# Kernel optimization log

Hardware: AMD Instinct MI355X
Metric: run time of the kernel (lower is better)

Reference implementation:

```python
import jax, jax.numpy as jnp
import numpy as np

N = 10000      # num_nodes
E = 320000     # num_edges
B = 8          # batch
S = 12         # seq_length
H = 64         # hidden_channels
HEADS = 4
C = H // HEADS # per-head dim = 16
L = 3          # num_layers
P = 3          # pred_length
EPS = 1e-5


def setup_inputs():
    key = jax.random.key(0)
    ks = jax.random.split(key, 20)
    g = lambda k, sh, s=0.05: jax.random.normal(k, sh, dtype=jnp.float32) * s
    return {
        "x": jax.random.normal(ks[0], (B, S, N), dtype=jnp.float32),
        "edge_index": jax.random.randint(ks[1], (2, E), 0, N, dtype=jnp.int64),
        "in_W": g(ks[2], (S, H), 0.2), "in_b": g(ks[3], (H,)),
        "Wq": g(ks[4], (L, H, H), 0.1), "bq": g(ks[5], (L, H)),
        "Wk": g(ks[6], (L, H, H), 0.1), "bk": g(ks[7], (L, H)),
        "Wv": g(ks[8], (L, H, H), 0.1), "bv": g(ks[9], (L, H)),
        "Wsk": g(ks[10], (L, H, H), 0.1), "bsk": g(ks[11], (L, H)),
        "ln_g": jnp.ones((H,), jnp.float32), "ln_b": jnp.zeros((H,), jnp.float32),
        "out_W": g(ks[12], (H, P), 0.1), "out_b": g(ks[13], (P,)),
    }


def _layer_norm(x, g, b):
    mu = x.mean(-1, keepdims=True)
    var = ((x - mu) ** 2).mean(-1, keepdims=True)
    return (x - mu) * jax.lax.rsqrt(var + EPS) * g + b


def _transformer_conv(x, src, dst, Wq, bq, Wk, bk, Wv, bv, Wsk, bsk):
    # x: [N, H]; PyG TransformerConv, concat=True, root_weight=True, beta=False
    n = x.shape[0]
    q = (x @ Wq + bq).reshape(n, HEADS, C)
    k = (x @ Wk + bk).reshape(n, HEADS, C)
    v = (x @ Wv + bv).reshape(n, HEADS, C)
    # messages flow src -> dst; attention logits per edge per head
    logits = (q[dst] * k[src]).sum(-1) / np.sqrt(C)           # [E, HEADS]
    m = jax.ops.segment_max(logits, dst, num_segments=n)       # [N, HEADS]
    e = jnp.exp(logits - m[dst])
    den = jax.ops.segment_sum(e, dst, num_segments=n)          # [N, HEADS]
    a = e / den[dst]                                           # [E, HEADS]
    agg = jax.ops.segment_sum(a[..., None] * v[src], dst, num_segments=n)
    return agg.reshape(n, H) + x @ Wsk + bsk


def reference(x, edge_index, in_W, in_b, Wq, bq, Wk, bk, Wv, bv, Wsk, bsk,
              ln_g, ln_b, out_W, out_b):
    src, dst = edge_index[0], edge_index[1]
    h = jnp.einsum('bsn,sh->bnh', x, in_W) + in_b              # [B, N, H]
    for l in range(L):
        conv = jax.vmap(lambda xb: _transformer_conv(
            xb, src, dst, Wq[l], bq[l], Wk[l], bk[l],
            Wv[l], bv[l], Wsk[l], bsk[l]))(h)
        h = _layer_norm(h + conv, ln_g, ln_b)                  # dropout: eval mode
    out = h @ out_W + out_b                                    # [B, N, P]
    return out.transpose(0, 2, 1)                              # [B, P, N]
```

## Files before the change

### kernel.cpp

```cpp
#include <hip/hip_runtime.h>
#include <hip/hip_bf16.h>
#include <math.h>

#define NN 10000
#define EE 320000
#define BB 8
#define SS 12
#define PP 3
#define LL 3
#define BN (BB*NN)
#define CSR_CAP (EE + 16*NN + 64)
#define QSCL (0.25f * 1.44269504f)

typedef __attribute__((ext_vector_type(8))) short bf8_t;
typedef __attribute__((ext_vector_type(4))) float f4_t;

__device__ __forceinline__ float bf2f(unsigned short u) {
    unsigned int x = ((unsigned int)u) << 16;
    return __builtin_bit_cast(float, x);
}
__device__ __forceinline__ unsigned short f2bf(float f) {
    unsigned int u = __builtin_bit_cast(unsigned int, f);
    u += 0x7FFF + ((u >> 16) & 1);
    return (unsigned short)(u >> 16);
}
__device__ __forceinline__ unsigned short f2h(float f) {
    _Float16 h = (_Float16)f;
    return __builtin_bit_cast(unsigned short, h);
}
__device__ __forceinline__ float dot2(unsigned a, unsigned b, float c) {
    float d;
    asm("v_dot2_f32_f16 %0, %1, %2, %3" : "=v"(d) : "v"(a), "v"(b), "v"(c));
    return d;
}
__device__ __forceinline__ float fma_mixlo(unsigned v, float w, float acc) {
    float d;
    asm("v_fma_mix_f32 %0, %1, %2, %3 op_sel_hi:[1,0,0]"
        : "=v"(d) : "v"(v), "v"(w), "v"(acc));
    return d;
}
__device__ __forceinline__ float fma_mixhi(unsigned v, float w, float acc) {
    float d;
    asm("v_fma_mix_f32 %0, %1, %2, %3 op_sel:[1,0,0] op_sel_hi:[1,0,0]"
        : "=v"(d) : "v"(v), "v"(w), "v"(acc));
    return d;
}
template<int CTRL>
__device__ __forceinline__ float dppadd(float x) {
    int t = __builtin_amdgcn_update_dpp(0, __builtin_bit_cast(int, x), CTRL, 0xF, 0xF, true);
    return x + __builtin_bit_cast(float, t);
}
#define QX1 0xB1
#define QX2 0x4E
#define RR4 0x124
#define RR8 0x128
__device__ __forceinline__ float quad_sum(float x) {
    x = dppadd<QX1>(x); x = dppadd<QX2>(x); return x;
}
__device__ __forceinline__ float row_sum(float x) {
    x = dppadd<QX1>(x); x = dppadd<QX2>(x);
    x = dppadd<RR4>(x); x = dppadd<RR8>(x); return x;
}

__global__ __launch_bounds__(256) void k_count(const int* __restrict__ ei, int* __restrict__ cnt,
                                               const float* __restrict__ Wq, const float* __restrict__ Wk,
                                               const float* __restrict__ Wv, const float* __restrict__ Ws,
                                               const float* __restrict__ bq, const float* __restrict__ bk,
                                               const float* __restrict__ bv, const float* __restrict__ bs,
                                               unsigned short* __restrict__ wtb, float* __restrict__ bprep) {
    int e = blockIdx.x * 256 + threadIdx.x;
    if (e < EE) atomicAdd(&cnt[ei[EE + e]], 1);
    if (e < LL * 4 * 64 * 64) {
        int l = e >> 14; int j = (e >> 12) & 3; int col = (e >> 6) & 63; int k = e & 63;
        const float* W = (j == 0 ? Wq : j == 1 ? Wk : j == 2 ? Wv : Ws) + l * 4096;
        float v = W[k * 64 + col];
        if (j == 0) v *= QSCL;
        wtb[e] = f2bf(v);
    }
    if (e < LL * 4 * 64) {
        int l = e >> 8; int j = (e >> 6) & 3; int c = e & 63;
        const float* bsrc = (j == 0 ? bq : j == 1 ? bk : j == 2 ? bv : bs) + l * 64;
        bprep[e] = bsrc[c] * (j == 0 ? QSCL : 1.0f);
    }
}

__global__ __launch_bounds__(1024) void k_scan(int* __restrict__ cnt,
                                               int* __restrict__ rp,
                                               int* __restrict__ degv) {
    __shared__ int ssum[1024];
    int t = threadIdx.x;
    int base = t * 10;
    int loc[10];
    int s = 0;
#pragma unroll
    for (int j = 0; j < 10; ++j) {
        int i = base + j;
        int d = (i < NN) ? cnt[i] : 0;
        loc[j] = d;
        s += (d + 15) & ~15;
    }
    ssum[t] = s;
    __syncthreads();
    for (int off = 1; off < 1024; off <<= 1) {
        int v = (t >= off) ? ssum[t - off] : 0;
        __syncthreads();
        ssum[t] += v;
        __syncthreads();
    }
    int run = ssum[t] - s;
#pragma unroll
    for (int j = 0; j < 10; ++j) {
        int i = base + j;
        if (i < NN) {
            rp[i]   = run;
            degv[i] = loc[j];
            cnt[i]  = run;
            run += (loc[j] + 15) & ~15;
        }
    }
}

__global__ __launch_bounds__(256) void k_fill(const int* __restrict__ ei, int* __restrict__ cursor,
                                              int* __restrict__ csr) {
    int e = blockIdx.x * 256 + threadIdx.x;
    if (e >= EE) return;
    int dst = ei[EE + e];
    int pos = atomicAdd(&cursor[dst], 1);
    csr[pos] = ei[e] << 8;
}

__global__ __launch_bounds__(256, 4) void k_gemm(const float* __restrict__ x,
                                                 const float* __restrict__ inW,
                                                 const float* __restrict__ inb,
                                                 int first,
                                                 unsigned short* hb,
                                                 float* h,
                                                 const unsigned short* __restrict__ wtb,
                                                 const float* __restrict__ bprep,
                                                 unsigned short* __restrict__ qh,
                                                 unsigned short* __restrict__ kv) {
    int tid = threadIdx.x;
    int l = tid & 63, w = tid >> 6;
    int row0 = blockIdx.x * 64;
    int colb = l & 15, kg = l >> 4, rquad = kg;

    if (first) {
        int c = tid & 63;
        int rb = tid >> 6;
        for (int j = 0; j < 16; ++j) {
            int row = row0 + rb + j * 4;
            int b = row / NN;
            int n = row - b * NN;
            float s = inb[c];
#pragma unroll
            for (int t = 0; t < SS; ++t)
                s += x[((size_t)b * SS + t) * NN + n] * inW[t * 64 + c];
            h[(size_t)row * 64 + c]  = s;
            hb[(size_t)row * 64 + c] = f2bf(s);
        }
        __syncthreads();
    }

    const unsigned short* wb = wtb + (size_t)w * 4096;
    bf8_t wfr[2][4];
#pragma unroll
    for (int ks = 0; ks < 2; ++ks)
#pragma unroll
        for (int ct = 0; ct < 4; ++ct)
            wfr[ks][ct] = *(const bf8_t*)(wb + (ct * 16 + colb) * 64 + ks * 32 + kg * 8);
    float4 biasv[4];
#pragma unroll
    for (int ct = 0; ct < 4; ++ct)
        biasv[ct] = *(const float4*)(bprep + w * 64 + ct * 16 + rquad * 4);

#pragma unroll
    for (int rt = 0; rt < 4; ++rt) {
        bf8_t hfr[2];
#pragma unroll
        for (int ks = 0; ks < 2; ++ks)
            hfr[ks] = *(const bf8_t*)(hb + (size_t)(row0 + rt * 16 + colb) * 64 + ks * 32 + kg * 8);
        f4_t acc[4];
#pragma unroll
        for (int ct = 0; ct < 4; ++ct) acc[ct] = (f4_t){0.f, 0.f, 0.f, 0.f};
#pragma unroll
        for (int ks = 0; ks < 2; ++ks)
#pragma unroll
            for (int ct = 0; ct < 4; ++ct)
                acc[ct] = __builtin_amdgcn_mfma_f32_16x16x32_bf16(wfr[ks][ct], hfr[ks], acc[ct], 0, 0, 0);

        int rowid = row0 + rt * 16 + colb;
        size_t rowoff = (size_t)rowid * 64;
#pragma unroll
        for (int ct = 0; ct < 4; ++ct) {
            int c0 = ct * 16 + rquad * 4;
            float v0 = acc[ct][0] + biasv[ct].x;
            float v1 = acc[ct][1] + biasv[ct].y;
            float v2 = acc[ct][2] + biasv[ct].z;
            float v3 = acc[ct][3] + biasv[ct].w;
            if (w == 0) {
                ushort4 st = {f2h(v0), f2h(v1), f2h(v2), f2h(v3)};
                *(ushort4*)(qh + rowoff + c0) = st;
            } else if (w == 1) {
                ushort4 st = {f2h(v0), f2h(v1), f2h(v2), f2h(v3)};
                *(ushort4*)(kv + (size_t)rowid * 128 + ((c0 >> 2) << 3)) = st;
            } else if (w == 2) {
                ushort4 st = {f2h(v0), f2h(v1), f2h(v2), f2h(v3)};
                *(ushort4*)(kv + (size_t)rowid * 128 + ((c0 >> 2) << 3) + 4) = st;
            } else {
                float4 hv = *(float4*)(h + rowoff + c0);
                hv.x += v0; hv.y += v1; hv.z += v2; hv.w += v3;
                *(float4*)(h + rowoff + c0) = hv;
            }
        }
    }
}

__global__ __launch_bounds__(256, 8) void k_attn_ln(const unsigned short* __restrict__ qh,
                                                    const unsigned short* __restrict__ kv,
                                                    const int* __restrict__ rp,
                                                    const int* __restrict__ degv,
                                                    const int* __restrict__ csr,
                                                    const float* __restrict__ lng,
                                                    const float* __restrict__ lnb,
                                                    float* __restrict__ h,
                                                    unsigned short* __restrict__ hb,
                                                    const float* __restrict__ oW,
                                                    const float* __restrict__ ob,
                                                    float* __restrict__ out) {
    int b    = blockIdx.x & 7;
    int n    = ((blockIdx.x >> 3) << 2) | __builtin_amdgcn_readfirstlane(threadIdx.x >> 6);
    int lane = threadIdx.x & 63;
    int lg   = lane & 15;
    int grp  = lane >> 4;
    size_t wid = (size_t)b * NN + n;

    const char* kvbase = (const char*)kv + (size_t)b * NN * 256;
    int lgoff = lg * 16;

    uint2 qp = ((const uint2*)qh)[wid * 16 + lg];

    int e0 = rp[n], deg = degv[n];
    int nf  = deg >> 4;
    int rem = deg & 15;
    float den0 = 0.f, den1 = 0.f;
    float4 av0 = {0.f, 0.f, 0.f, 0.f}, av1 = {0.f, 0.f, 0.f, 0.f};

    int e = e0;
    for (int f = 0; f < nf; ++f, e += 16) {
        int4 cc = *(const int4*)(csr + e + grp * 4);
        unsigned o0 = (unsigned)(cc.x + lgoff);
        unsigned o1 = (unsigned)(cc.y + lgoff);
        unsigned o2 = (unsigned)(cc.z + lgoff);
        unsigned o3 = (unsigned)(cc.w + lgoff);
        uint4 a0 = *(const uint4*)(kvbase + o0);
        uint4 a1 = *(const uint4*)(kvbase + o1);
        uint4 a2 = *(const uint4*)(kvbase + o2);
        uint4 a3 = *(const uint4*)(kvbase + o3);

        float d0 = dot2(a0.y, qp.y, dot2(a0.x, qp.x, 0.f));
        float d1 = dot2(a1.y, qp.y, dot2(a1.x, qp.x, 0.f));
        float d2 = dot2(a2.y, qp.y, dot2(a2.x, qp.x, 0.f));
        float d3 = dot2(a3.y, qp.y, dot2(a3.x, qp.x, 0.f));
        d0 = quad_sum(d0); d1 = quad_sum(d1);
        d2 = quad_sum(d2); d3 = quad_sum(d3);

        float w0 = __builtin_amdgcn_exp2f(d0);
        float w1 = __builtin_amdgcn_exp2f(d1);
        float w2 = __builtin_amdgcn_exp2f(d2);
        float w3 = __builtin_amdgcn_exp2f(d3);

        den0 += w0 + w1;
        den1 += w2 + w3;
        av0.x = fma_mixlo(a0.z, w0, av0.x); av0.x = fma_mixlo(a1.z, w1, av0.x);
        av0.y = fma_mixhi(a0.z, w0, av0.y); av0.y = fma_mixhi(a1.z, w1, av0.y);
        av0.z = fma_mixlo(a0.w, w0, av0.z); av0.z = fma_mixlo(a1.w, w1, av0.z);
        av0.w = fma_mixhi(a0.w, w0, av0.w); av0.w = fma_mixhi(a1.w, w1, av0.w);
        av1.x = fma_mixlo(a2.z, w2, av1.x); av1.x = fma_mixlo(a3.z, w3, av1.x);
        av1.y = fma_mixhi(a2.z, w2, av1.y); av1.y = fma_mixhi(a3.z, w3, av1.y);
        av1.z = fma_mixlo(a2.w, w2, av1.z); av1.z = fma_mixlo(a3.w, w3, av1.z);
        av1.w = fma_mixhi(a2.w, w2, av1.w); av1.w = fma_mixhi(a3.w, w3, av1.w);
    }
    if (rem) {
        int4 cc = *(const int4*)(csr + e + grp * 4);
        unsigned o0 = (unsigned)(cc.x + lgoff);
        unsigned o1 = (unsigned)(cc.y + lgoff);
        unsigned o2 = (unsigned)(cc.z + lgoff);
        unsigned o3 = (unsigned)(cc.w + lgoff);
        uint4 a0 = *(const uint4*)(kvbase + o0);
        uint4 a1 = *(const uint4*)(kvbase + o1);
        uint4 a2 = *(const uint4*)(kvbase + o2);
        uint4 a3 = *(const uint4*)(kvbase + o3);

        int eb = grp * 4;
        float m0 = (eb + 0 < rem) ? 1.f : 0.f;
        float m1 = (eb + 1 < rem) ? 1.f : 0.f;
        float m2 = (eb + 2 < rem) ? 1.f : 0.f;
        float m3 = (eb + 3 < rem) ? 1.f : 0.f;

        float d0 = dot2(a0.y, qp.y, dot2(a0.x, qp.x, 0.f));
        float d1 = dot2(a1.y, qp.y, dot2(a1.x, qp.x, 0.f));
        float d2 = dot2(a2.y, qp.y, dot2(a2.x, qp.x, 0.f));
        float d3 = dot2(a3.y, qp.y, dot2(a3.x, qp.x, 0.f));
        d0 = quad_sum(d0); d1 = quad_sum(d1);
        d2 = quad_sum(d2); d3 = quad_sum(d3);

        float w0 = m0 * __builtin_amdgcn_exp2f(d0);
        float w1 = m1 * __builtin_amdgcn_exp2f(d1);
        float w2 = m2 * __builtin_amdgcn_exp2f(d2);
        float w3 = m3 * __builtin_amdgcn_exp2f(d3);

        den0 += w0 + w1;
        den1 += w2 + w3;
        av0.x = fma_mixlo(a0.z, w0, av0.x); av0.x = fma_mixlo(a1.z, w1, av0.x);
        av0.y = fma_mixhi(a0.z, w0, av0.y); av0.y = fma_mixhi(a1.z, w1, av0.y);
        av0.z = fma_mixlo(a0.w, w0, av0.z); av0.z = fma_mixlo(a1.w, w1, av0.z);
        av0.w = fma_mixhi(a0.w, w0, av0.w); av0.w = fma_mixhi(a1.w, w1, av0.w);
        av1.x = fma_mixlo(a2.z, w2, av1.x); av1.x = fma_mixlo(a3.z, w3, av1.x);
        av1.y = fma_mixhi(a2.z, w2, av1.y); av1.y = fma_mixhi(a3.z, w3, av1.y);
        av1.z = fma_mixlo(a2.w, w2, av1.z); av1.z = fma_mixlo(a3.w, w3, av1.z);
        av1.w = fma_mixhi(a2.w, w2, av1.w); av1.w = fma_mixhi(a3.w, w3, av1.w);
    }

    float den = den0 + den1;
    float4 av = {av0.x + av1.x, av0.y + av1.y, av0.z + av1.z, av0.w + av1.w};

#pragma unroll
    for (int off = 16; off <= 32; off <<= 1) {
        den  += __shfl_xor(den, off);
        av.x += __shfl_xor(av.x, off); av.y += __shfl_xor(av.y, off);
        av.z += __shfl_xor(av.z, off); av.w += __shfl_xor(av.w, off);
    }
    float inv = (den > 0.f) ? __builtin_amdgcn_rcpf(den) : 0.f;

    float4 h4 = ((const float4*)h)[wid * 16 + lg];
    float4 x4;
    x4.x = h4.x + av.x * inv; x4.y = h4.y + av.y * inv;
    x4.z = h4.z + av.z * inv; x4.w = h4.w + av.w * inv;

    float s = row_sum(x4.x + x4.y + x4.z + x4.w);
    float mu = s * (1.f / 64.f);
    float4 dx;
    dx.x = x4.x - mu; dx.y = x4.y - mu; dx.z = x4.z - mu; dx.w = x4.w - mu;
    float vs = row_sum(dx.x * dx.x + dx.y * dx.y + dx.z * dx.z + dx.w * dx.w);
    float r = __builtin_amdgcn_rsqf(vs * (1.f / 64.f) + 1e-5f);

    float4 g4 = ((const float4*)lng)[lg];
    float4 b4 = ((const float4*)lnb)[lg];
    float4 o4;
    o4.x = dx.x * r * g4.x + b4.x; o4.y = dx.y * r * g4.y + b4.y;
    o4.z = dx.z * r * g4.z + b4.z; o4.w = dx.w * r * g4.w + b4.w;

    if (oW) {
        int c0 = lg * 4;
        float t0 = o4.x * oW[(c0+0)*3+0] + o4.y * oW[(c0+1)*3+0] + o4.z * oW[(c0+2)*3+0] + o4.w * oW[(c0+3)*3+0];
        float t1 = o4.x * oW[(c0+0)*3+1] + o4.y * oW[(c0+1)*3+1] + o4.z * oW[(c0+2)*3+1] + o4.w * oW[(c0+3)*3+1];
        float t2 = o4.x * oW[(c0+0)*3+2] + o4.y * oW[(c0+1)*3+2] + o4.z * oW[(c0+2)*3+2] + o4.w * oW[(c0+3)*3+2];
        t0 = row_sum(t0); t1 = row_sum(t1); t2 = row_sum(t2);
        if (lane == 0) {
            out[((size_t)b * PP + 0) * NN + n] = t0 + ob[0];
            out[((size_t)b * PP + 1) * NN + n] = t1 + ob[1];
            out[((size_t)b * PP + 2) * NN + n] = t2 + ob[2];
        }
    } else if (lane < 16) {
        ((float4*)h)[wid * 16 + lg] = o4;
        ushort4 hu = {f2bf(o4.x), f2bf(o4.y), f2bf(o4.z), f2bf(o4.w)};
        ((ushort4*)hb)[wid * 16 + lg] = hu;
    }
}

extern "C" void kernel_launch(void* const* d_in, const int* in_sizes, int n_in,
                              void* d_out, int out_size, void* d_ws, size_t ws_size,
                              hipStream_t stream) {
    const float* x    = (const float*)d_in[0];
    const int*   ei   = (const int*)  d_in[1];
    const float* inW  = (const float*)d_in[2];
    const float* inb  = (const float*)d_in[3];
    const float* Wq   = (const float*)d_in[4];
    const float* bq   = (const float*)d_in[5];
    const float* Wk   = (const float*)d_in[6];
    const float* bk   = (const float*)d_in[7];
    const float* Wv   = (const float*)d_in[8];
    const float* bv   = (const float*)d_in[9];
    const float* Wsk  = (const float*)d_in[10];
    const float* bsk  = (const float*)d_in[11];
    const float* lng  = (const float*)d_in[12];
    const float* lnb  = (const float*)d_in[13];
    const float* outW = (const float*)d_in[14];
    const float* outb = (const float*)d_in[15];
    float* out = (float*)d_out;

    float* h    = (float*)d_ws;
    unsigned short* hb = (unsigned short*)(h + (size_t)BN * 64);
    unsigned short* qh = hb + (size_t)BN * 64;
    unsigned short* kv = qh + (size_t)BN * 64;
    int* rp      = (int*)(kv + (size_t)BN * 128);
    int* degv    = rp + NN;
    int* cursor  = degv + NN;
    int* csr     = cursor + NN;
    unsigned short* wtb = (unsigned short*)(csr + CSR_CAP);
    float* bprep = (float*)(wtb + LL * 4 * 64 * 64);

    hipMemsetAsync(cursor, 0, (NN + CSR_CAP) * sizeof(int), stream);
    k_count<<<(EE + 255) / 256, 256, 0, stream>>>(ei, cursor, Wq, Wk, Wv, Wsk,
                                                  bq, bk, bv, bsk, wtb, bprep);
    k_scan <<<1, 1024, 0, stream>>>(cursor, rp, degv);
    k_fill <<<(EE + 255) / 256, 256, 0, stream>>>(ei, cursor, csr);

    for (int l = 0; l < LL; ++l) {
        k_gemm<<<BN / 64, 256, 0, stream>>>(x, inW, inb, (l == 0) ? 1 : 0, hb, h,
                                            wtb + (size_t)l * 4 * 4096,
                                            bprep + (size_t)l * 4 * 64, qh, kv);
        k_attn_ln<<<BN / 4, 256, 0, stream>>>(qh, kv, rp, degv, csr,
                                              lng, lnb, h, hb,
                                              (l == LL - 1) ? outW : nullptr, outb, out);
    }
}
```

Baseline: 286.5 us.

## Software-pipeline edge gathers in attention kernel and shrink blocks to two waves

The attention loop now issues the next 16-edge chunk's CSR and K/V gathers before computing the current chunk, so gather latency overlaps with the dot/exp/accumulate work. The tail chunk is folded into the same pipeline with masking. Blocks shrink from 256 to 128 threads (two nodes per block, twice as many blocks) and the launch bound changes to (128,6). Holding a second set of loaded registers raises register pressure, and the new bound may limit occupancy.

Measured after the change: 287.1 us. Within noise of the previous version (+0.2%).

```diff
diff --git a/kernel.cpp b/kernel.cpp
--- a/kernel.cpp
+++ b/kernel.cpp
@@ -215,7 +215,31 @@
     }
 }
 
-__global__ __launch_bounds__(256, 8) void k_attn_ln(const unsigned short* __restrict__ qh,
+#define EDGE_COMPUTE(A0, A1, A2, A3, M0, M1, M2, M3)                               \
+    {                                                                              \
+        float d0 = dot2(A0.y, qp.y, dot2(A0.x, qp.x, 0.f));                        \
+        float d1 = dot2(A1.y, qp.y, dot2(A1.x, qp.x, 0.f));                        \
+        float d2 = dot2(A2.y, qp.y, dot2(A2.x, qp.x, 0.f));                        \
+        float d3 = dot2(A3.y, qp.y, dot2(A3.x, qp.x, 0.f));                        \
+        d0 = quad_sum(d0); d1 = quad_sum(d1);                                      \
+        d2 = quad_sum(d2); d3 = quad_sum(d3);                                      \
+        float w0 = M0 * __builtin_amdgcn_exp2f(d0);                                \
+        float w1 = M1 * __builtin_amdgcn_exp2f(d1);                                \
+        float w2 = M2 * __builtin_amdgcn_exp2f(d2);                                \
+        float w3 = M3 * __builtin_amdgcn_exp2f(d3);                                \
+        den0 += w0 + w1;                                                           \
+        den1 += w2 + w3;                                                           \
+        av0.x = fma_mixlo(A0.z, w0, av0.x); av0.x = fma_mixlo(A1.z, w1, av0.x);    \
+        av0.y = fma_mixhi(A0.z, w0, av0.y); av0.y = fma_mixhi(A1.z, w1, av0.y);    \
+        av0.z = fma_mixlo(A0.w, w0, av0.z); av0.z = fma_mixlo(A1.w, w1, av0.z);    \
+        av0.w = fma_mixhi(A0.w, w0, av0.w); av0.w = fma_mixhi(A1.w, w1, av0.w);    \
+        av1.x = fma_mixlo(A2.z, w2, av1.x); av1.x = fma_mixlo(A3.z, w3, av1.x);    \
+        av1.y = fma_mixhi(A2.z, w2, av1.y); av1.y = fma_mixhi(A3.z, w3, av1.y);    \
+        av1.z = fma_mixlo(A2.w, w2, av1.z); av1.z = fma_mixlo(A3.w, w3, av1.z);    \
+        av1.w = fma_mixhi(A2.w, w2, av1.w); av1.w = fma_mixhi(A3.w, w3, av1.w);    \
+    }
+
+__global__ __launch_bounds__(128, 6) void k_attn_ln(const unsigned short* __restrict__ qh,
                                                     const unsigned short* __restrict__ kv,
                                                     const int* __restrict__ rp,
                                                     const int* __restrict__ degv,
@@ -228,7 +252,7 @@
                                                     const float* __restrict__ ob,
                                                     float* __restrict__ out) {
     int b    = blockIdx.x & 7;
-    int n    = ((blockIdx.x >> 3) << 2) | __builtin_amdgcn_readfirstlane(threadIdx.x >> 6);
+    int n    = ((blockIdx.x >> 3) << 1) | __builtin_amdgcn_readfirstlane(threadIdx.x >> 6);
     int lane = threadIdx.x & 63;
     int lg   = lane & 15;
     int grp  = lane >> 4;
@@ -240,85 +264,38 @@
     uint2 qp = ((const uint2*)qh)[wid * 16 + lg];
 
     int e0 = rp[n], deg = degv[n];
-    int nf  = deg >> 4;
-    int rem = deg & 15;
+    int nf   = deg >> 4;
+    int rem  = deg & 15;
+    int ntot = nf + (rem ? 1 : 0);
     float den0 = 0.f, den1 = 0.f;
     float4 av0 = {0.f, 0.f, 0.f, 0.f}, av1 = {0.f, 0.f, 0.f, 0.f};
 
-    int e = e0;
-    for (int f = 0; f < nf; ++f, e += 16) {
-        int4 cc = *(const int4*)(csr + e + grp * 4);
-        unsigned o0 = (unsigned)(cc.x + lgoff);
-        unsigned o1 = (unsigned)(cc.y + lgoff);
-        unsigned o2 = (unsigned)(cc.z + lgoff);
-        unsigned o3 = (unsigned)(cc.w + lgoff);
-        uint4 a0 = *(const uint4*)(kvbase + o0);
-        uint4 a1 = *(const uint4*)(kvbase + o1);
-        uint4 a2 = *(const uint4*)(kvbase + o2);
-        uint4 a3 = *(const uint4*)(kvbase + o3);
-
-        float d0 = dot2(a0.y, qp.y, dot2(a0.x, qp.x, 0.f));
-        float d1 = dot2(a1.y, qp.y, dot2(a1.x, qp.x, 0.f));
-        float d2 = dot2(a2.y, qp.y, dot2(a2.x, qp.x, 0.f));
-        float d3 = dot2(a3.y, qp.y, dot2(a3.x, qp.x, 0.f));
-        d0 = quad_sum(d0); d1 = quad_sum(d1);
-        d2 = quad_sum(d2); d3 = quad_sum(d3);
-
-        float w0 = __builtin_amdgcn_exp2f(d0);
-        float w1 = __builtin_amdgcn_exp2f(d1);
-        float w2 = __builtin_amdgcn_exp2f(d2);
-        float w3 = __builtin_amdgcn_exp2f(d3);
-
-        den0 += w0 + w1;
-        den1 += w2 + w3;
-        av0.x = fma_mixlo(a0.z, w0, av0.x); av0.x = fma_mixlo(a1.z, w1, av0.x);
-        av0.y = fma_mixhi(a0.z, w0, av0.y); av0.y = fma_mixhi(a1.z, w1, av0.y);
-        av0.z = fma_mixlo(a0.w, w0, av0.z); av0.z = fma_mixlo(a1.w, w1, av0.z);
-        av0.w = fma_mixhi(a0.w, w0, av0.w); av0.w = fma_mixhi(a1.w, w1, av0.w);
-        av1.x = fma_mixlo(a2.z, w2, av1.x); av1.x = fma_mixlo(a3.z, w3, av1.x);
-        av1.y = fma_mixhi(a2.z, w2, av1.y); av1.y = fma_mixhi(a3.z, w3, av1.y);
-        av1.z = fma_mixlo(a2.w, w2, av1.z); av1.z = fma_mixlo(a3.w, w3, av1.z);
-        av1.w = fma_mixhi(a2.w, w2, av1.w); av1.w = fma_mixhi(a3.w, w3, av1.w);
-    }
-    if (rem) {
-        int4 cc = *(const int4*)(csr + e + grp * 4);
-        unsigned o0 = (unsigned)(cc.x + lgoff);
-        unsigned o1 = (unsigned)(cc.y + lgoff);
-        unsigned o2 = (unsigned)(cc.z + lgoff);
-        unsigned o3 = (unsigned)(cc.w + lgoff);
-        uint4 a0 = *(const uint4*)(kvbase + o0);
-        uint4 a1 = *(const uint4*)(kvbase + o1);
-        uint4 a2 = *(const uint4*)(kvbase + o2);
-        uint4 a3 = *(const uint4*)(kvbase + o3);
-
+    if (ntot > 0) {
+        const int* cp = csr + e0 + grp * 4;
+        int4 cc = *(const int4*)cp;
+        uint4 a0 = *(const uint4*)(kvbase + (unsigned)(cc.x + lgoff));
+        uint4 a1 = *(const uint4*)(kvbase + (unsigned)(cc.y + lgoff));
+        uint4 a2 = *(const uint4*)(kvbase + (unsigned)(cc.z + lgoff));
+        uint4 a3 = *(const uint4*)(kvbase + (unsigned)(cc.w + lgoff));
+
+        for (int f = 1; f < ntot; ++f) {
+            int4 ccn = *(const int4*)(cp + (f << 4));
+            uint4 b0 = *(const uint4*)(kvbase + (unsigned)(ccn.x + lgoff));
+            uint4 b1 = *(const uint4*)(kvbase + (unsigned)(ccn.y + lgoff));
+            uint4 b2 = *(const uint4*)(kvbase + (unsigned)(ccn.z + lgoff));
+            uint4 b3 = *(const uint4*)(kvbase + (unsigned)(ccn.w + lgoff));
+
+            EDGE_COMPUTE(a0, a1, a2, a3, 1.f, 1.f, 1.f, 1.f);
+
+            a0 = b0; a1 = b1; a2 = b2; a3 = b3;
+        }
+        int remm = rem ? rem : 16;
         int eb = grp * 4;
-        float m0 = (eb + 0 < rem) ? 1.f : 0.f;
-        float m1 = (eb + 1 < rem) ? 1.f : 0.f;
-        float m2 = (eb + 2 < rem) ? 1.f : 0.f;
-        float m3 = (eb + 3 < rem) ? 1.f : 0.f;
-
-        float d0 = dot2(a0.y, qp.y, dot2(a0.x, qp.x, 0.f));
-        float d1 = dot2(a1.y, qp.y, dot2(a1.x, qp.x, 0.f));
-        float d2 = dot2(a2.y, qp.y, dot2(a2.x, qp.x, 0.f));
-        float d3 = dot2(a3.y, qp.y, dot2(a3.x, qp.x, 0.f));
-        d0 = quad_sum(d0); d1 = quad_sum(d1);
-        d2 = quad_sum(d2); d3 = quad_sum(d3);
-
-        float w0 = m0 * __builtin_amdgcn_exp2f(d0);
-        float w1 = m1 * __builtin_amdgcn_exp2f(d1);
-        float w2 = m2 * __builtin_amdgcn_exp2f(d2);
-        float w3 = m3 * __builtin_amdgcn_exp2f(d3);
-
-        den0 += w0 + w1;
-        den1 += w2 + w3;
-        av0.x = fma_mixlo(a0.z, w0, av0.x); av0.x = fma_mixlo(a1.z, w1, av0.x);
-        av0.y = fma_mixhi(a0.z, w0, av0.y); av0.y = fma_mixhi(a1.z, w1, av0.y);
-        av0.z = fma_mixlo(a0.w, w0, av0.z); av0.z = fma_mixlo(a1.w, w1, av0.z);
-        av0.w = fma_mixhi(a0.w, w0, av0.w); av0.w = fma_mixhi(a1.w, w1, av0.w);
-        av1.x = fma_mixlo(a2.z, w2, av1.x); av1.x = fma_mixlo(a3.z, w3, av1.x);
-        av1.y = fma_mixhi(a2.z, w2, av1.y); av1.y = fma_mixhi(a3.z, w3, av1.y);
-        av1.z = fma_mixlo(a2.w, w2, av1.z); av1.z = fma_mixlo(a3.w, w3, av1.z);
-        av1.w = fma_mixhi(a2.w, w2, av1.w); av1.w = fma_mixhi(a3.w, w3, av1.w);
+        float m0 = (eb + 0 < remm) ? 1.f : 0.f;
+        float m1 = (eb + 1 < remm) ? 1.f : 0.f;
+        float m2 = (eb + 2 < remm) ? 1.f : 0.f;
+        float m3 = (eb + 3 < remm) ? 1.f : 0.f;
+        EDGE_COMPUTE(a0, a1, a2, a3, m0, m1, m2, m3);
     }
 
     float den = den0 + den1;
@@ -410,7 +387,7 @@
         k_gemm<<<BN / 64, 256, 0, stream>>>(x, inW, inb, (l == 0) ? 1 : 0, hb, h,
                                             wtb + (size_t)l * 4 * 4096,
                                             bprep + (size_t)l * 4 * 64, qh, kv);
-        k_attn_ln<<<BN / 4, 256, 0, stream>>>(qh, kv, rp, degv, csr,
+        k_attn_ln<<<BN / 2, 128, 0, stream>>>(qh, kv, rp, degv, csr,
                                               lng, lnb, h, hb,
                                               (l == LL - 1) ? outW : nullptr, outb, out);
     }
```
